# Performance work log

Hardware: AMD Instinct MI355X
Metric: run time of the kernel (lower is better)

The kernel has to match this reference:

```python
import jax, jax.numpy as jnp
import numpy as np

B, S, D_MODEL, D_FF, N_EXPERTS, TOP_K = 4, 4096, 512, 2048, 8, 2


def setup_inputs() -> dict:
    key = jax.random.key(0)
    k1, k2, k3, k4 = jax.random.split(key, 4)
    hidden_states = jax.random.normal(k1, (B, S, D_MODEL), dtype=jnp.float32)
    gate_w = jax.random.normal(k2, (N_EXPERTS, D_MODEL), dtype=jnp.float32) * 0.02
    w1 = jax.random.normal(k3, (N_EXPERTS, D_FF, D_MODEL), dtype=jnp.float32) * (1.0 / np.sqrt(D_MODEL))
    w2 = jax.random.normal(k4, (N_EXPERTS, D_MODEL, D_FF), dtype=jnp.float32) * 0.02
    return {"hidden_states": hidden_states, "gate_w": gate_w, "w1": w1, "w2": w2}


def reference(hidden_states, gate_w, w1, w2):
    b, s, d = hidden_states.shape
    t = b * s
    n_experts = w1.shape[0]
    flat = hidden_states.reshape(t, d)                         # [T, D]

    # Router
    router_logits = flat @ gate_w.T                            # [T, E]
    routing_probs = jax.nn.softmax(router_logits, axis=-1)
    routing_weights, selected_experts = jax.lax.top_k(routing_probs, TOP_K)
    routing_weights = routing_weights / routing_weights.sum(axis=-1, keepdims=True)

    # Dense all-expert FFN (eval mode: dropout is identity). GELU exact (erf), as nn.GELU default.
    h = jax.nn.gelu(jnp.einsum('td,efd->tef', flat, w1), approximate=False)  # [T, E, d_ff]
    expert_outputs = jnp.einsum('tef,egf->teg', h, w2)         # [T, E, D]

    # scatter_add routing weights into dense [T, E] matrix, then weighted combine
    ewm = jnp.zeros((t, n_experts), dtype=flat.dtype)
    ewm = ewm.at[jnp.arange(t)[:, None], selected_experts].add(routing_weights)
    combined = jnp.einsum('te,ted->td', ewm, expert_outputs)   # [T, D]
    output = combined.reshape(b, s, d)

    # entropy regularization loss
    log_probs = jnp.log(jnp.clip(routing_probs, 1e-6))
    entropy_loss = (-(routing_probs * log_probs).sum(axis=-1)).mean()

    return output, router_logits, entropy_loss
```

## Files before the change

### kernel.cpp

```cpp
#include <hip/hip_runtime.h>
#include <hip/hip_bf16.h>
#include <math.h>

#define T_TOKENS 16384
#define DM 512
#define DFF 2048
#define NE 8
#define TOKT 64
#define FCH 256
#define NFC (DFF / FCH)

#define RL_OFF  ((size_t)T_TOKENS * DM)
#define ENT_OFF (RL_OFF + (size_t)T_TOKENS * NE)

typedef __attribute__((ext_vector_type(8))) short short8;
typedef __attribute__((ext_vector_type(4))) float f32x4;

__device__ __forceinline__ unsigned short f2bf(float f) {
    union { float f; unsigned u; } v; v.f = f;
    unsigned r = v.u + 0x7FFFu + ((v.u >> 16) & 1u);
    return (unsigned short)(r >> 16);
}
__device__ __forceinline__ float bf2f(unsigned short h) {
    union { unsigned u; float f; } v; v.u = ((unsigned)h) << 16; return v.f;
}
__device__ __forceinline__ void atomAddF(float* p, float v) {
    __hip_atomic_fetch_add(p, v, __ATOMIC_RELAXED, __HIP_MEMORY_SCOPE_AGENT);
}

__global__ void cvt_kernel(const float* __restrict__ src, unsigned short* __restrict__ dst, size_t n4) {
    for (size_t i = blockIdx.x * (size_t)blockDim.x + threadIdx.x; i < n4;
         i += (size_t)gridDim.x * blockDim.x) {
        f32x4 v = ((const f32x4*)src)[i];
        unsigned short b0 = f2bf(v.x), b1 = f2bf(v.y), b2 = f2bf(v.z), b3 = f2bf(v.w);
        ((unsigned long long*)dst)[i] =
            (unsigned long long)b0 | ((unsigned long long)b1 << 16) |
            ((unsigned long long)b2 << 32) | ((unsigned long long)b3 << 48);
    }
}

__global__ __launch_bounds__(1024)
void router_kernel(const float* __restrict__ x, const float* __restrict__ gw,
                   float* __restrict__ out, int* __restrict__ cursor,
                   int* __restrict__ slotlist, float* __restrict__ wgtlist,
                   float* __restrict__ entPartial) {
    __shared__ int   lcnt[NE];
    __shared__ int   lbase[NE];
    __shared__ float lent[16];
    __shared__ int   le[16][2];
    __shared__ int   lpos[16][2];
    __shared__ float lw[16][2];

    int tid = threadIdx.x;
    int wid = tid >> 6, lane = tid & 63;
    int t = blockIdx.x * 16 + wid;
    if (tid < NE) lcnt[tid] = 0;
    __syncthreads();

    const float* xr = x + (size_t)t * DM + lane * 8;
    f32x4 x0 = *(const f32x4*)xr;
    f32x4 x1 = *(const f32x4*)(xr + 4);

    float logit[NE];
#pragma unroll
    for (int e = 0; e < NE; ++e) {
        const float* g = gw + e * DM + lane * 8;
        f32x4 g0 = *(const f32x4*)g;
        f32x4 g1 = *(const f32x4*)(g + 4);
        float p = x0.x*g0.x + x0.y*g0.y + x0.z*g0.z + x0.w*g0.w
                + x1.x*g1.x + x1.y*g1.y + x1.z*g1.z + x1.w*g1.w;
#pragma unroll
        for (int off = 32; off > 0; off >>= 1) p += __shfl_xor(p, off);
        logit[e] = p;
    }
    float m = logit[0];
#pragma unroll
    for (int e = 1; e < NE; ++e) m = fmaxf(m, logit[e]);
    float pr[NE]; float s = 0.f;
#pragma unroll
    for (int e = 0; e < NE; ++e) { pr[e] = expf(logit[e] - m); s += pr[e]; }
    float inv = 1.f / s;
    float ent = 0.f;
#pragma unroll
    for (int e = 0; e < NE; ++e) { pr[e] *= inv; ent -= pr[e] * logf(fmaxf(pr[e], 1e-6f)); }
    float p0 = -1.f, p1 = -1.f; int e0 = 0, e1 = 0;
#pragma unroll
    for (int e = 0; e < NE; ++e) {
        float p = pr[e];
        if (p > p0)      { p1 = p0; e1 = e0; p0 = p; e0 = e; }
        else if (p > p1) { p1 = p;  e1 = e; }
    }
    float wsum = p0 + p1;

    if (lane == 0) {
        lent[wid] = ent;
        le[wid][0] = e0; le[wid][1] = e1;
        lw[wid][0] = p0 / wsum; lw[wid][1] = p1 / wsum;
        lpos[wid][0] = atomicAdd(&lcnt[e0], 1);
        lpos[wid][1] = atomicAdd(&lcnt[e1], 1);
    }
    float myLogit = 0.f;
#pragma unroll
    for (int e = 0; e < NE; ++e) if (lane == e) myLogit = logit[e];
    if (lane < NE) out[RL_OFF + (size_t)t * NE + lane] = myLogit;

    __syncthreads();
    if (tid < NE) lbase[tid] = atomicAdd(cursor + tid, lcnt[tid]);
    __syncthreads();
    if (tid < 16) {
        int a0 = le[tid][0], a1 = le[tid][1];
        int tt = blockIdx.x * 16 + tid;
        int q0 = lbase[a0] + lpos[tid][0];
        int q1 = lbase[a1] + lpos[tid][1];
        slotlist[a0 * T_TOKENS + q0] = tt * 2;     wgtlist[a0 * T_TOKENS + q0] = lw[tid][0];
        slotlist[a1 * T_TOKENS + q1] = tt * 2 + 1; wgtlist[a1 * T_TOKENS + q1] = lw[tid][1];
    }
    if (tid == 0) {
        float sum = 0.f;
#pragma unroll
        for (int w = 0; w < 16; ++w) sum += lent[w];
        entPartial[blockIdx.x] = sum;
    }
}

__global__ void ent_reduce(const float* __restrict__ part, float* __restrict__ out) {
    __shared__ float s[16];
    int tid = threadIdx.x;
    float v = part[tid];
#pragma unroll
    for (int off = 32; off > 0; off >>= 1) v += __shfl_xor(v, off);
    if ((tid & 63) == 0) s[tid >> 6] = v;
    __syncthreads();
    if (tid == 0) {
        float tot = 0.f;
#pragma unroll
        for (int w = 0; w < 16; ++w) tot += s[w];
        out[ENT_OFF] = tot * (1.0f / T_TOKENS);
    }
}

template <int XB, int SLOT>
__global__ __launch_bounds__(512, 2)
void ffn_kernel(const float* __restrict__ x, const unsigned short* __restrict__ xb,
                const unsigned short* __restrict__ w1b, const unsigned short* __restrict__ w2b,
                const int* __restrict__ cursor, const int* __restrict__ slotlist,
                const float* __restrict__ wgtlist,
                unsigned short* __restrict__ ybuf, float* __restrict__ out) {
    __shared__ unsigned short Xs[TOKT * DM];
    __shared__ unsigned short Hs[TOKT * FCH];

    int e   = blockIdx.x & 7;
    int cnt = cursor[e];
    int tid = threadIdx.x;
    int wid = tid >> 6, lane = tid & 63;
    int l16 = lane & 15, lg = lane >> 4;

    const unsigned short* w1e = w1b + (size_t)e * DFF * DM;
    const unsigned short* w2e = w2b + (size_t)e * DM * DFF;
    const int*   sl = slotlist + e * T_TOKENS;
    const float* wl = wgtlist  + e * T_TOKENS;

    int step = (gridDim.x >> 3) * TOKT;
#pragma unroll 1
    for (int t0 = (blockIdx.x >> 3) * TOKT; t0 < cnt; t0 += step) {
#pragma unroll
        for (int it = 0; it < 8; ++it) {
            int u = tid + it * 512;
            int row = u >> 6, c16 = u & 63;
            int idx = t0 + row;
            int entry = sl[(idx < cnt) ? idx : t0];
            int t = entry >> 1;
            short8 v;
            if constexpr (XB == 1) {
                v = *(const short8*)(xb + (size_t)t * DM + c16 * 8);
            } else {
                const float* src = x + (size_t)t * DM + c16 * 8;
                f32x4 a = *(const f32x4*)src, b = *(const f32x4*)(src + 4);
                v[0]=(short)f2bf(a.x); v[1]=(short)f2bf(a.y); v[2]=(short)f2bf(a.z); v[3]=(short)f2bf(a.w);
                v[4]=(short)f2bf(b.x); v[5]=(short)f2bf(b.y); v[6]=(short)f2bf(b.z); v[7]=(short)f2bf(b.w);
            }
            *(short8*)((char*)Xs + row * 1024 + ((c16 << 4) ^ ((row & 7) << 4))) = v;
        }
        __syncthreads();

        f32x4 Yacc[4][4] = {};

#pragma unroll 1
        for (int fc = 0; fc < NFC; ++fc) {
            f32x4 Hacc[4][2] = {};
            const unsigned short* w1p0 = w1e + (size_t)(fc * FCH + wid * 32 + l16) * DM + lg * 8;
            const unsigned short* w1p1 = w1p0 + (size_t)16 * DM;
#pragma unroll
            for (int ks = 0; ks < 16; ++ks) {
                short8 B0 = *(const short8*)(w1p0 + ks * 32);
                short8 B1 = *(const short8*)(w1p1 + ks * 32);
#pragma unroll
                for (int rt = 0; rt < 4; ++rt) {
                    int row = rt * 16 + l16;
                    short8 A = *(const short8*)((const char*)Xs + row * 1024 +
                                ((ks * 64 + lg * 16) ^ ((row & 7) << 4)));
                    Hacc[rt][0] = __builtin_amdgcn_mfma_f32_16x16x32_bf16(A, B0, Hacc[rt][0], 0, 0, 0);
                    Hacc[rt][1] = __builtin_amdgcn_mfma_f32_16x16x32_bf16(A, B1, Hacc[rt][1], 0, 0, 0);
                }
            }
            __syncthreads();
#pragma unroll
            for (int rt = 0; rt < 4; ++rt)
#pragma unroll
            for (int ct = 0; ct < 2; ++ct)
#pragma unroll
            for (int r = 0; r < 4; ++r) {
                float h = Hacc[rt][ct][r];
                float g = 0.5f * h * (1.0f + erff(h * 0.70710678118f));
                int row = rt * 16 + lg * 4 + r;
                int colb = (wid * 32 + ct * 16 + l16) * 2;
                *(unsigned short*)((char*)Hs + row * 512 + (colb ^ ((row & 7) << 4))) = f2bf(g);
            }
            __syncthreads();
            const unsigned short* w2p = w2e + (size_t)(wid * 64 + l16) * DFF + fc * FCH + lg * 8;
#pragma unroll
            for (int ks = 0; ks < 8; ++ks) {
                short8 B[4];
#pragma unroll
                for (int ct = 0; ct < 4; ++ct)
                    B[ct] = *(const short8*)(w2p + (size_t)ct * 16 * DFF + ks * 32);
#pragma unroll
                for (int rt = 0; rt < 4; ++rt) {
                    int row = rt * 16 + l16;
                    short8 A = *(const short8*)((const char*)Hs + row * 512 +
                                ((ks * 64 + lg * 16) ^ ((row & 7) << 4)));
#pragma unroll
                    for (int ct = 0; ct < 4; ++ct)
                        Yacc[rt][ct] = __builtin_amdgcn_mfma_f32_16x16x32_bf16(A, B[ct], Yacc[rt][ct], 0, 0, 0);
                }
            }
        }
#pragma unroll
        for (int rt = 0; rt < 4; ++rt)
#pragma unroll
        for (int r = 0; r < 4; ++r) {
            int row = rt * 16 + lg * 4 + r;
            int idx = t0 + row;
            if (idx < cnt) {
                int entry = sl[idx];
                float wgt = wl[idx];
                if constexpr (SLOT == 1) {
                    unsigned short* dst = ybuf + (size_t)entry * DM + wid * 64;
#pragma unroll
                    for (int ct = 0; ct < 4; ++ct)
                        dst[ct * 16 + l16] = f2bf(Yacc[rt][ct][r] * wgt);
                } else {
                    float* dst = out + (size_t)(entry >> 1) * DM + wid * 64;
#pragma unroll
                    for (int ct = 0; ct < 4; ++ct)
                        atomAddF(dst + ct * 16 + l16, Yacc[rt][ct][r] * wgt);
                }
            }
        }
        __syncthreads();
    }
}

__global__ __launch_bounds__(256)
void combine_kernel(const unsigned short* __restrict__ ybuf, float* __restrict__ out) {
    int gid = blockIdx.x * 256 + threadIdx.x;
    int t = gid >> 6, c8 = (gid & 63) * 8;
    const unsigned short* r0 = ybuf + ((size_t)t * 2) * DM + c8;
    short8 a = *(const short8*)r0;
    short8 b = *(const short8*)(r0 + DM);
    float* o = out + (size_t)t * DM + c8;
    f32x4 v0, v1;
    v0.x = bf2f((unsigned short)a[0]) + bf2f((unsigned short)b[0]);
    v0.y = bf2f((unsigned short)a[1]) + bf2f((unsigned short)b[1]);
    v0.z = bf2f((unsigned short)a[2]) + bf2f((unsigned short)b[2]);
    v0.w = bf2f((unsigned short)a[3]) + bf2f((unsigned short)b[3]);
    v1.x = bf2f((unsigned short)a[4]) + bf2f((unsigned short)b[4]);
    v1.y = bf2f((unsigned short)a[5]) + bf2f((unsigned short)b[5]);
    v1.z = bf2f((unsigned short)a[6]) + bf2f((unsigned short)b[6]);
    v1.w = bf2f((unsigned short)a[7]) + bf2f((unsigned short)b[7]);
    *(f32x4*)o = v0;
    *(f32x4*)(o + 4) = v1;
}

extern "C" void kernel_launch(void* const* d_in, const int* in_sizes, int n_in,
                              void* d_out, int out_size, void* d_ws, size_t ws_size,
                              hipStream_t stream) {
    const float* x  = (const float*)d_in[0];
    const float* gw = (const float*)d_in[1];
    const float* w1 = (const float*)d_in[2];
    const float* w2 = (const float*)d_in[3];
    float* out = (float*)d_out;
    char* ws = (char*)d_ws;

    const size_t W1N = (size_t)NE * DFF * DM;
    const size_t W2N = (size_t)NE * DM * DFF;
    unsigned short* w1b = (unsigned short*)ws;
    unsigned short* w2b = w1b + W1N;
    size_t off = (W1N + W2N) * 2;
    int*   cursor   = (int*)(ws + off);   off += 256;
    int*   slotlist = (int*)(ws + off);   off += (size_t)NE * T_TOKENS * 4;
    float* wgtlist  = (float*)(ws + off); off += (size_t)NE * T_TOKENS * 4;
    float* entPart  = (float*)(ws + off); off += 8192;
    unsigned short* xbb = (unsigned short*)(ws + off); off += (size_t)T_TOKENS * DM * 2;
    size_t needB = off;
    unsigned short* ybuf = (unsigned short*)(ws + off); off += (size_t)T_TOKENS * 2 * DM * 2;
    size_t needA = off;

    int tier = (ws_size >= needA) ? 2 : ((ws_size >= needB) ? 1 : 0);

    hipMemsetAsync(cursor, 0, 64, stream);
    if (tier < 2) hipMemsetAsync(out, 0, RL_OFF * sizeof(float), stream);

    cvt_kernel<<<2048, 256, 0, stream>>>(w1, w1b, W1N / 4);
    cvt_kernel<<<2048, 256, 0, stream>>>(w2, w2b, W2N / 4);
    if (tier >= 1) cvt_kernel<<<2048, 256, 0, stream>>>(x, xbb, (size_t)T_TOKENS * DM / 4);

    router_kernel<<<T_TOKENS / 16, 1024, 0, stream>>>(x, gw, out, cursor, slotlist, wgtlist, entPart);
    ent_reduce<<<1, 1024, 0, stream>>>(entPart, out);

    if (tier == 2) {
        ffn_kernel<1, 1><<<NE * 64, 512, 0, stream>>>(x, xbb, w1b, w2b, cursor, slotlist, wgtlist, ybuf, out);
        combine_kernel<<<(T_TOKENS * DM / 8) / 256, 256, 0, stream>>>(ybuf, out);
    } else if (tier == 1) {
        ffn_kernel<1, 0><<<NE * 64, 512, 0, stream>>>(x, xbb, w1b, w2b, cursor, slotlist, wgtlist, nullptr, out);
    } else {
        ffn_kernel<0, 0><<<NE * 64, 512, 0, stream>>>(x, nullptr, w1b, w2b, cursor, slotlist, wgtlist, nullptr, out);
    }
}
```

Before: 527.3 us.

## Software-pipeline expert weight loads and transpose GEMM1 for packed GELU stores

The FFN kernel now prefetches W1 fragments three k-steps ahead and W2 fragments two k-steps ahead in registers, including across chunk boundaries. This hides global-memory latency behind the MFMA work. GEMM1 operand roles are swapped (weights as A, tokens as B), so each lane owns four consecutive d_ff values and can write the GELU result to shared memory as one packed 64-bit store instead of scalar 16-bit stores. Routing weights are staged in shared memory. The prefetch buffers raise register pressure, which may hurt occupancy at the 512x2 launch bounds.

```diff
diff --git a/kernel.cpp b/kernel.cpp
--- a/kernel.cpp
+++ b/kernel.cpp
@@ -146,14 +146,17 @@
                 const int* __restrict__ cursor, const int* __restrict__ slotlist,
                 const float* __restrict__ wgtlist,
                 unsigned short* __restrict__ ybuf, float* __restrict__ out) {
-    __shared__ unsigned short Xs[TOKT * DM];
-    __shared__ unsigned short Hs[TOKT * FCH];
+    __shared__ char XsB[TOKT * DM * 2];
+    __shared__ char HsB[TOKT * FCH * 2];
+    __shared__ int   tIdx[TOKT];
+    __shared__ float tW[TOKT];
 
     int e   = blockIdx.x & 7;
     int cnt = cursor[e];
     int tid = threadIdx.x;
     int wid = tid >> 6, lane = tid & 63;
     int l16 = lane & 15, lg = lane >> 4;
+    int swz = (l16 & 7) << 4;
 
     const unsigned short* w1e = w1b + (size_t)e * DFF * DM;
     const unsigned short* w2e = w2b + (size_t)e * DM * DFF;
@@ -163,13 +166,19 @@
     int step = (gridDim.x >> 3) * TOKT;
 #pragma unroll 1
     for (int t0 = (blockIdx.x >> 3) * TOKT; t0 < cnt; t0 += step) {
+        if (tid < TOKT) {
+            int i = t0 + tid;
+            int src = (i < cnt) ? i : t0;
+            tIdx[tid] = sl[src] >> 1;
+            tW[tid]   = (i < cnt) ? wl[i] : 0.f;
+        }
 #pragma unroll
         for (int it = 0; it < 8; ++it) {
             int u = tid + it * 512;
             int row = u >> 6, c16 = u & 63;
             int idx = t0 + row;
-            int entry = sl[(idx < cnt) ? idx : t0];
-            int t = entry >> 1;
+            int sidx = (idx < cnt) ? idx : t0;
+            int t = sl[sidx] >> 1;
             short8 v;
             if constexpr (XB == 1) {
                 v = *(const short8*)(xb + (size_t)t * DM + c16 * 8);
@@ -179,81 +188,112 @@
                 v[0]=(short)f2bf(a.x); v[1]=(short)f2bf(a.y); v[2]=(short)f2bf(a.z); v[3]=(short)f2bf(a.w);
                 v[4]=(short)f2bf(b.x); v[5]=(short)f2bf(b.y); v[6]=(short)f2bf(b.z); v[7]=(short)f2bf(b.w);
             }
-            *(short8*)((char*)Xs + row * 1024 + ((c16 << 4) ^ ((row & 7) << 4))) = v;
+            *(short8*)(XsB + row * 1024 + ((c16 << 4) ^ ((row & 7) << 4))) = v;
         }
         __syncthreads();
 
         f32x4 Yacc[4][4] = {};
+        const unsigned short* w1base = w1e + (size_t)(wid * 32 + l16) * DM + lg * 8;
+        const unsigned short* w2base = w2e + (size_t)(wid * 64 + l16) * DFF + lg * 8;
+
+        short8 Ap[3][2];
+#pragma unroll
+        for (int k = 0; k < 3; ++k) {
+            Ap[k][0] = *(const short8*)(w1base + k * 32);
+            Ap[k][1] = *(const short8*)(w1base + 16 * DM + k * 32);
+        }
 
 #pragma unroll 1
         for (int fc = 0; fc < NFC; ++fc) {
-            f32x4 Hacc[4][2] = {};
-            const unsigned short* w1p0 = w1e + (size_t)(fc * FCH + wid * 32 + l16) * DM + lg * 8;
-            const unsigned short* w1p1 = w1p0 + (size_t)16 * DM;
+            const unsigned short* w1f = w1base + (size_t)fc * FCH * DM;
+            f32x4 Hacc[2][4] = {};
 #pragma unroll
             for (int ks = 0; ks < 16; ++ks) {
-                short8 B0 = *(const short8*)(w1p0 + ks * 32);
-                short8 B1 = *(const short8*)(w1p1 + ks * 32);
-#pragma unroll
-                for (int rt = 0; rt < 4; ++rt) {
-                    int row = rt * 16 + l16;
-                    short8 A = *(const short8*)((const char*)Xs + row * 1024 +
-                                ((ks * 64 + lg * 16) ^ ((row & 7) << 4)));
-                    Hacc[rt][0] = __builtin_amdgcn_mfma_f32_16x16x32_bf16(A, B0, Hacc[rt][0], 0, 0, 0);
-                    Hacc[rt][1] = __builtin_amdgcn_mfma_f32_16x16x32_bf16(A, B1, Hacc[rt][1], 0, 0, 0);
-                }
-            }
+                short8 a0 = Ap[ks % 3][0], a1 = Ap[ks % 3][1];
+                if (ks < 13) {
+                    Ap[ks % 3][0] = *(const short8*)(w1f + (ks + 3) * 32);
+                    Ap[ks % 3][1] = *(const short8*)(w1f + 16 * DM + (ks + 3) * 32);
+                }
+#pragma unroll
+                for (int tt = 0; tt < 4; ++tt) {
+                    short8 xf = *(const short8*)(XsB + (tt * 16 + l16) * 1024 +
+                                                 ((ks * 64 + lg * 16) ^ swz));
+                    Hacc[0][tt] = __builtin_amdgcn_mfma_f32_16x16x32_bf16(a0, xf, Hacc[0][tt], 0, 0, 0);
+                    Hacc[1][tt] = __builtin_amdgcn_mfma_f32_16x16x32_bf16(a1, xf, Hacc[1][tt], 0, 0, 0);
+                }
+            }
+            if (fc + 1 < NFC) {
+                const unsigned short* w1n = w1base + (size_t)(fc + 1) * FCH * DM;
+#pragma unroll
+                for (int k = 0; k < 3; ++k) {
+                    Ap[k][0] = *(const short8*)(w1n + k * 32);
+                    Ap[k][1] = *(const short8*)(w1n + 16 * DM + k * 32);
+                }
+            }
+            const unsigned short* w2f = w2base + fc * FCH;
+            short8 Bp[2][4];
+#pragma unroll
+            for (int k = 0; k < 2; ++k)
+#pragma unroll
+                for (int gt = 0; gt < 4; ++gt)
+                    Bp[k][gt] = *(const short8*)(w2f + (size_t)gt * 16 * DFF + k * 32);
+
             __syncthreads();
 #pragma unroll
-            for (int rt = 0; rt < 4; ++rt)
-#pragma unroll
-            for (int ct = 0; ct < 2; ++ct)
-#pragma unroll
-            for (int r = 0; r < 4; ++r) {
-                float h = Hacc[rt][ct][r];
-                float g = 0.5f * h * (1.0f + erff(h * 0.70710678118f));
-                int row = rt * 16 + lg * 4 + r;
-                int colb = (wid * 32 + ct * 16 + l16) * 2;
-                *(unsigned short*)((char*)Hs + row * 512 + (colb ^ ((row & 7) << 4))) = f2bf(g);
+            for (int ft = 0; ft < 2; ++ft)
+#pragma unroll
+            for (int tt = 0; tt < 4; ++tt) {
+                f32x4 h = Hacc[ft][tt];
+                unsigned long long pk = 0;
+#pragma unroll
+                for (int r = 0; r < 4; ++r) {
+                    float g = 0.5f * h[r] * (1.0f + erff(h[r] * 0.70710678118f));
+                    pk |= (unsigned long long)f2bf(g) << (r * 16);
+                }
+                int token = tt * 16 + l16;
+                int f2 = wid * 64 + ft * 32 + lg * 8;
+                *(unsigned long long*)(HsB + token * 512 + (f2 ^ swz)) = pk;
             }
             __syncthreads();
-            const unsigned short* w2p = w2e + (size_t)(wid * 64 + l16) * DFF + fc * FCH + lg * 8;
 #pragma unroll
             for (int ks = 0; ks < 8; ++ks) {
-                short8 B[4];
-#pragma unroll
-                for (int ct = 0; ct < 4; ++ct)
-                    B[ct] = *(const short8*)(w2p + (size_t)ct * 16 * DFF + ks * 32);
-#pragma unroll
-                for (int rt = 0; rt < 4; ++rt) {
-                    int row = rt * 16 + l16;
-                    short8 A = *(const short8*)((const char*)Hs + row * 512 +
-                                ((ks * 64 + lg * 16) ^ ((row & 7) << 4)));
-#pragma unroll
-                    for (int ct = 0; ct < 4; ++ct)
-                        Yacc[rt][ct] = __builtin_amdgcn_mfma_f32_16x16x32_bf16(A, B[ct], Yacc[rt][ct], 0, 0, 0);
-                }
-            }
-        }
-#pragma unroll
-        for (int rt = 0; rt < 4; ++rt)
+                short8 b0 = Bp[ks & 1][0], b1 = Bp[ks & 1][1];
+                short8 b2 = Bp[ks & 1][2], b3 = Bp[ks & 1][3];
+                if (ks < 6) {
+#pragma unroll
+                    for (int gt = 0; gt < 4; ++gt)
+                        Bp[ks & 1][gt] = *(const short8*)(w2f + (size_t)gt * 16 * DFF + (ks + 2) * 32);
+                }
+#pragma unroll
+                for (int tt = 0; tt < 4; ++tt) {
+                    short8 af = *(const short8*)(HsB + (tt * 16 + l16) * 512 +
+                                                 ((ks * 64 + lg * 16) ^ swz));
+                    Yacc[tt][0] = __builtin_amdgcn_mfma_f32_16x16x32_bf16(af, b0, Yacc[tt][0], 0, 0, 0);
+                    Yacc[tt][1] = __builtin_amdgcn_mfma_f32_16x16x32_bf16(af, b1, Yacc[tt][1], 0, 0, 0);
+                    Yacc[tt][2] = __builtin_amdgcn_mfma_f32_16x16x32_bf16(af, b2, Yacc[tt][2], 0, 0, 0);
+                    Yacc[tt][3] = __builtin_amdgcn_mfma_f32_16x16x32_bf16(af, b3, Yacc[tt][3], 0, 0, 0);
+                }
+            }
+        }
+#pragma unroll
+        for (int tt = 0; tt < 4; ++tt)
 #pragma unroll
         for (int r = 0; r < 4; ++r) {
-            int row = rt * 16 + lg * 4 + r;
+            int row = tt * 16 + lg * 4 + r;
             int idx = t0 + row;
             if (idx < cnt) {
                 int entry = sl[idx];
-                float wgt = wl[idx];
+                float wgt = tW[row];
                 if constexpr (SLOT == 1) {
                     unsigned short* dst = ybuf + (size_t)entry * DM + wid * 64;
 #pragma unroll
-                    for (int ct = 0; ct < 4; ++ct)
-                        dst[ct * 16 + l16] = f2bf(Yacc[rt][ct][r] * wgt);
+                    for (int gt = 0; gt < 4; ++gt)
+                        dst[gt * 16 + l16] = f2bf(Yacc[tt][gt][r] * wgt);
                 } else {
                     float* dst = out + (size_t)(entry >> 1) * DM + wid * 64;
 #pragma unroll
-                    for (int ct = 0; ct < 4; ++ct)
-                        atomAddF(dst + ct * 16 + l16, Yacc[rt][ct][r] * wgt);
+                    for (int gt = 0; gt < 4; ++gt)
+                        atomAddF(dst + gt * 16 + l16, Yacc[tt][gt][r] * wgt);
                 }
             }
         }
```

Result: faster. 515.1 us (-2.3%).
